# Kernel optimization log

Hardware: AMD Instinct MI355X
Metric: run time of the kernel (lower is better)

Reference implementation:

```python
import jax, jax.numpy as jnp
import numpy as np

D_MODEL = 1024
HEADS = 16
D_K = D_MODEL // HEADS
D_FF = 4 * D_MODEL
EPS = 1e-6


def setup_inputs() -> dict:
    key = jax.random.key(0)
    ks = jax.random.split(key, 8)
    B, S = 2, 2048
    x = jax.random.normal(ks[0], (B, S, D_MODEL), dtype=jnp.float32)
    mask = jnp.tril(jnp.ones((S, S), dtype=jnp.float32))  # causal mask
    sd = 1.0 / np.sqrt(D_MODEL)
    Wq = jax.random.normal(ks[1], (D_MODEL, D_MODEL), dtype=jnp.float32) * sd
    Wk = jax.random.normal(ks[2], (D_MODEL, D_MODEL), dtype=jnp.float32) * sd
    Wv = jax.random.normal(ks[3], (D_MODEL, D_MODEL), dtype=jnp.float32) * sd
    Wo = jax.random.normal(ks[4], (D_MODEL, D_MODEL), dtype=jnp.float32) * sd
    W1 = jax.random.normal(ks[5], (D_FF, D_MODEL), dtype=jnp.float32) * sd  # torch Linear weight [out,in]
    W2 = jax.random.normal(ks[6], (D_MODEL, D_FF), dtype=jnp.float32) * (1.0 / np.sqrt(D_FF))
    g1 = jnp.ones((D_MODEL,), dtype=jnp.float32)
    b1 = jnp.zeros((D_MODEL,), dtype=jnp.float32)
    g2 = jnp.ones((D_MODEL,), dtype=jnp.float32)
    b2 = jnp.zeros((D_MODEL,), dtype=jnp.float32)
    return dict(x=x, mask=mask, Wq=Wq, Wk=Wk, Wv=Wv, Wo=Wo, W1=W1, W2=W2,
                g1=g1, b1=b1, g2=g2, b2=b2)


def _layernorm(x, gamma, beta):
    mean = jnp.mean(x, axis=-1, keepdims=True)
    var = jnp.var(x, axis=-1, keepdims=True, ddof=1)  # torch.var is unbiased
    return gamma * (x - mean) / jnp.sqrt(var + EPS) + beta


def reference(x, mask, Wq, Wk, Wv, Wo, W1, W2, g1, b1, g2, b2):
    B, S, D = x.shape
    def split_heads(t):
        return t.reshape(B, S, HEADS, D_K).transpose(0, 2, 1, 3)  # [B,H,S,dk]
    q = split_heads(x @ Wq.T)
    k = split_heads(x @ Wk.T)
    v = split_heads(x @ Wv.T)
    scores = jnp.einsum('bhqd,bhkd->bhqk', q, k) / np.sqrt(D_K)
    scores = jnp.where(mask == 0, -jnp.inf, scores)
    weights = jax.nn.softmax(scores, axis=-1)
    attn = jnp.einsum('bhqk,bhkd->bhqd', weights, v)
    attn = attn.transpose(0, 2, 1, 3).reshape(B, S, D) @ Wo.T
    x = _layernorm(x + attn, g1, b1)
    ff = jax.nn.relu(x @ W1.T) @ W2.T
    return _layernorm(x + ff, g2, b2)
```

## Files before the change

### kernel.cpp

```cpp
#include <hip/hip_runtime.h>

typedef __attribute__((ext_vector_type(8))) short short8;
typedef __attribute__((ext_vector_type(4))) float f32x4;
typedef unsigned short u16;

#define DEV static __device__ __forceinline__

DEV float b2f(u16 u) { union { unsigned u; float f; } c; c.u = ((unsigned)u) << 16; return c.f; }
DEV u16 f2b(float f) {
    union { float f; unsigned u; } c; c.f = f;
    unsigned u = c.u;
    u += 0x7fffu + ((u >> 16) & 1u);
    return (u16)(u >> 16);
}

DEV float wred_sum(float v) {
    #pragma unroll
    for (int o = 32; o > 0; o >>= 1) v += __shfl_xor(v, o, 64);
    return v;
}

DEV void glds16(const u16* g, u16* l) {
    __builtin_amdgcn_global_load_lds((const __attribute__((address_space(1))) void*)g,
                                     (__attribute__((address_space(3))) void*)l, 16, 0, 0);
}

__global__ __launch_bounds__(256) void cast_all(const float* __restrict__ x,
                                                const float* __restrict__ Wq,
                                                const float* __restrict__ Wk,
                                                const float* __restrict__ Wv,
                                                const float* __restrict__ Wo,
                                                const float* __restrict__ W1,
                                                const float* __restrict__ W2,
                                                u16* __restrict__ xb,
                                                u16* __restrict__ wqkvb,
                                                u16* __restrict__ wob,
                                                u16* __restrict__ w1b,
                                                u16* __restrict__ w2b) {
    int blk = blockIdx.x;
    const float* src; u16* dst; int boff;
    if      (blk < 2048) { src = x;  dst = xb;              boff = blk; }
    else if (blk < 2560) { src = Wq; dst = wqkvb;           boff = blk - 2048; }
    else if (blk < 3072) { src = Wk; dst = wqkvb + 1048576; boff = blk - 2560; }
    else if (blk < 3584) { src = Wv; dst = wqkvb + 2097152; boff = blk - 3072; }
    else if (blk < 4096) { src = Wo; dst = wob;             boff = blk - 3584; }
    else if (blk < 6144) { src = W1; dst = w1b;             boff = blk - 4096; }
    else                 { src = W2; dst = w2b;             boff = blk - 6144; }
    int i = boff * 2048 + threadIdx.x * 8;
    float4 a = *(const float4*)(src + i);
    float4 b = *(const float4*)(src + i + 4);
    uint4 o;
    o.x = (unsigned)f2b(a.x) | ((unsigned)f2b(a.y) << 16);
    o.y = (unsigned)f2b(a.z) | ((unsigned)f2b(a.w) << 16);
    o.z = (unsigned)f2b(b.x) | ((unsigned)f2b(b.y) << 16);
    o.w = (unsigned)f2b(b.z) | ((unsigned)f2b(b.w) << 16);
    *(uint4*)(dst + i) = o;
}

template <int OUT_MODE>
__global__ __launch_bounds__(256) void gemm128(const u16* __restrict__ A,
                                               const u16* __restrict__ Bt,
                                               void* __restrict__ Cout,
                                               int M, int N, int Kd,
                                               int GMx, int GNx, int cxs) {
    __shared__ __attribute__((aligned(16))) u16 As[2][4096];
    __shared__ __attribute__((aligned(16))) u16 Bs[2][4096];

    const int tid  = threadIdx.x;
    const int wid  = tid >> 6;
    const int lane = tid & 63;
    const int quad = lane >> 4;
    const int l16  = lane & 15;
    const int wm   = wid & 1;
    const int wn   = wid >> 1;

    const int id  = blockIdx.x;
    const int xcd = id & 7;
    const int s   = id >> 3;
    const int xr  = xcd >> cxs;
    const int xc  = xcd & ((1 << cxs) - 1);
    const int nl  = s % GNx;
    const int ml  = s / GNx;
    const int m0  = (xr * GMx + ml) * 128;
    const int n0  = (xc * GNx + nl) * 128;

    const int c0 = tid, c1 = 256 + tid;
    const int mA0 = c0 >> 2, mA1 = c1 >> 2;
    const int kg0 = (c0 & 3) ^ ((mA0 ^ (mA0 >> 2)) & 3);
    const int kg1 = (c1 & 3) ^ ((mA1 ^ (mA1 >> 2)) & 3);
    const u16* ga0 = A  + (size_t)(m0 + mA0) * Kd + kg0 * 8;
    const u16* ga1 = A  + (size_t)(m0 + mA1) * Kd + kg1 * 8;
    const u16* gb0 = Bt + (size_t)(n0 + mA0) * Kd + kg0 * 8;
    const u16* gb1 = Bt + (size_t)(n0 + mA1) * Kd + kg1 * 8;

    f32x4 acc[4][4] = {};

    int mfr[4], nfr[4];
    #pragma unroll
    for (int t = 0; t < 4; ++t) {
        int m = wm * 64 + t * 16 + l16;
        mfr[t] = m * 32 + (quad ^ ((m ^ (m >> 2)) & 3)) * 8;
        int n = wn * 64 + t * 16 + l16;
        nfr[t] = n * 32 + (quad ^ ((n ^ (n >> 2)) & 3)) * 8;
    }

    #define STAGE(buf, kk)                                   \
        do {                                                 \
            glds16(ga0 + (kk), &As[buf][c0 * 8]);            \
            glds16(ga1 + (kk), &As[buf][c1 * 8]);            \
            glds16(gb0 + (kk), &Bs[buf][c0 * 8]);            \
            glds16(gb1 + (kk), &Bs[buf][c1 * 8]);            \
        } while (0)

    #define COMPUTE(buf)                                                      \
        do {                                                                  \
            short8 af[4], bf[4];                                              \
            _Pragma("unroll")                                                 \
            for (int t = 0; t < 4; ++t) af[t] = *(const short8*)&As[buf][mfr[t]]; \
            _Pragma("unroll")                                                 \
            for (int t = 0; t < 4; ++t) bf[t] = *(const short8*)&Bs[buf][nfr[t]]; \
            _Pragma("unroll")                                                 \
            for (int mt = 0; mt < 4; ++mt)                                    \
                _Pragma("unroll")                                             \
                for (int nt = 0; nt < 4; ++nt)                                \
                    acc[mt][nt] = __builtin_amdgcn_mfma_f32_16x16x32_bf16(af[mt], bf[nt], acc[mt][nt], 0, 0, 0); \
        } while (0)

    STAGE(0, 0);
    for (int k0 = 0; k0 < Kd; k0 += 64) {
        __syncthreads();
        STAGE(1, k0 + 32);
        COMPUTE(0);
        __syncthreads();
        if (k0 + 64 < Kd) STAGE(0, k0 + 64);
        COMPUTE(1);
    }
    #undef STAGE
    #undef COMPUTE

    #pragma unroll
    for (int mt = 0; mt < 4; ++mt) {
        #pragma unroll
        for (int nt = 0; nt < 4; ++nt) {
            #pragma unroll
            for (int r = 0; r < 4; ++r) {
                int row = m0 + wm * 64 + mt * 16 + quad * 4 + r;
                int col = n0 + wn * 64 + nt * 16 + l16;
                float v = acc[mt][nt][r];
                if (OUT_MODE == 1) v = fmaxf(v, 0.f);
                if (OUT_MODE == 2) {
                    ((float*)Cout)[(size_t)row * N + col] = v;
                } else {
                    ((u16*)Cout)[(size_t)row * N + col] = f2b(v);
                }
            }
        }
    }
}

#define QS 3072
__global__ __launch_bounds__(256) void attn_mfma(const u16* __restrict__ QKV,
                                                 u16* __restrict__ Om) {
    __shared__ __attribute__((aligned(16))) u16 K_sh[64][72];
    __shared__ __attribute__((aligned(16))) u16 V_sh[64][72];
    __shared__ __attribute__((aligned(16))) u16 P_sh[4][32][72];

    const int tid  = threadIdx.x;
    const int wid  = tid >> 6;
    const int lane = tid & 63;
    const int quad = lane >> 4;
    const int l16  = lane & 15;
    const int bh   = blockIdx.x & 31;
    const int b    = bh >> 4, h = bh & 15;
    const int qt   = 15 - (blockIdx.x >> 5);
    const int S = 2048, Dm = 1024;
    const int q0w = qt * 128 + wid * 32;

    const u16* Qm = QKV;
    const u16* Km = QKV + 1024;
    const u16* Vm = QKV + 2048;

    short8 bq[2][2];
    #pragma unroll
    for (int qs = 0; qs < 2; ++qs)
        #pragma unroll
        for (int dc = 0; dc < 2; ++dc)
            bq[qs][dc] = *(const short8*)(Qm + (size_t)(b * S + q0w + qs * 16 + l16) * QS
                                             + h * 64 + dc * 32 + quad * 8);

    float mS[2] = { -INFINITY, -INFINITY };
    float lS[2] = { 0.f, 0.f };
    f32x4 accO[4][2] = {};

    const int ntiles = qt * 2 + 2;
    for (int t = 0; t < ntiles; ++t) {
        const int k0 = t * 64;
        __syncthreads();
        #pragma unroll
        for (int it = 0; it < 2; ++it) {
            int key = (tid >> 3) + it * 32;
            int dcol = (tid & 7) * 8;
            *(uint4*)&K_sh[key][dcol] =
                *(const uint4*)(Km + (size_t)(b * S + k0 + key) * QS + h * 64 + dcol);
        }
        #pragma unroll
        for (int it = 0; it < 2; ++it) {
            int key = lane;
            int d0 = wid * 8 + it * 32;
            uint4 vv = *(const uint4*)(Vm + (size_t)(b * S + k0 + key) * QS + h * 64 + d0);
            const u16* ve = (const u16*)&vv;
            #pragma unroll
            for (int j = 0; j < 8; ++j) V_sh[d0 + j][key] = ve[j];
        }
        __syncthreads();

        if (k0 > q0w + 31) continue;

        f32x4 sC[4][2] = {};
        #pragma unroll
        for (int dc = 0; dc < 2; ++dc)
            #pragma unroll
            for (int st = 0; st < 4; ++st) {
                short8 ak = *(const short8*)&K_sh[st * 16 + l16][dc * 32 + quad * 8];
                #pragma unroll
                for (int qs = 0; qs < 2; ++qs)
                    sC[st][qs] = __builtin_amdgcn_mfma_f32_16x16x32_bf16(ak, bq[qs][dc], sC[st][qs], 0, 0, 0);
            }

        if (k0 + 63 > q0w) {
            #pragma unroll
            for (int st = 0; st < 4; ++st)
                #pragma unroll
                for (int qs = 0; qs < 2; ++qs)
                    #pragma unroll
                    for (int r = 0; r < 4; ++r) {
                        int key = k0 + st * 16 + quad * 4 + r;
                        int qq  = q0w + qs * 16 + l16;
                        sC[st][qs][r] = (key > qq) ? -INFINITY : sC[st][qs][r] * 0.125f;
                    }
        } else {
            #pragma unroll
            for (int st = 0; st < 4; ++st)
                #pragma unroll
                for (int qs = 0; qs < 2; ++qs)
                    #pragma unroll
                    for (int r = 0; r < 4; ++r) sC[st][qs][r] *= 0.125f;
        }

        #pragma unroll
        for (int qs = 0; qs < 2; ++qs) {
            float tmax = -INFINITY;
            #pragma unroll
            for (int st = 0; st < 4; ++st)
                #pragma unroll
                for (int r = 0; r < 4; ++r) tmax = fmaxf(tmax, sC[st][qs][r]);
            tmax = fmaxf(tmax, __shfl_xor(tmax, 16, 64));
            tmax = fmaxf(tmax, __shfl_xor(tmax, 32, 64));
            float mnew = fmaxf(mS[qs], tmax);
            float al = __expf(mS[qs] - mnew);
            mS[qs] = mnew;
            float rs = 0.f;
            #pragma unroll
            for (int st = 0; st < 4; ++st) {
                u16 pk[4];
                #pragma unroll
                for (int r = 0; r < 4; ++r) {
                    float p = __expf(sC[st][qs][r] - mnew);
                    rs += p;
                    pk[r] = f2b(p);
                }
                *(ushort4*)&P_sh[wid][qs * 16 + l16][st * 16 + quad * 4] =
                    make_ushort4(pk[0], pk[1], pk[2], pk[3]);
            }
            rs += __shfl_xor(rs, 16, 64);
            rs += __shfl_xor(rs, 32, 64);
            lS[qs] = lS[qs] * al + rs;
            #pragma unroll
            for (int dm = 0; dm < 4; ++dm)
                #pragma unroll
                for (int r = 0; r < 4; ++r) accO[dm][qs][r] *= al;
        }

        #pragma unroll
        for (int kc = 0; kc < 2; ++kc) {
            short8 bp[2];
            #pragma unroll
            for (int qs = 0; qs < 2; ++qs)
                bp[qs] = *(const short8*)&P_sh[wid][qs * 16 + l16][kc * 32 + quad * 8];
            #pragma unroll
            for (int dm = 0; dm < 4; ++dm) {
                short8 av = *(const short8*)&V_sh[dm * 16 + l16][kc * 32 + quad * 8];
                #pragma unroll
                for (int qs = 0; qs < 2; ++qs)
                    accO[dm][qs] = __builtin_amdgcn_mfma_f32_16x16x32_bf16(av, bp[qs], accO[dm][qs], 0, 0, 0);
            }
        }
    }

    __syncthreads();

    #pragma unroll
    for (int qs = 0; qs < 2; ++qs) {
        float rl = 1.f / lS[qs];
        #pragma unroll
        for (int dm = 0; dm < 4; ++dm) {
            u16 pk[4];
            #pragma unroll
            for (int r = 0; r < 4; ++r) pk[r] = f2b(accO[dm][qs][r] * rl);
            *(ushort4*)&P_sh[wid][qs * 16 + l16][dm * 16 + quad * 4] =
                make_ushort4(pk[0], pk[1], pk[2], pk[3]);
        }
    }
    __syncthreads();
    #pragma unroll
    for (int pass = 0; pass < 4; ++pass) {
        int qq = pass * 8 + (lane >> 3);
        int dd = (lane & 7) * 8;
        uint4 v = *(const uint4*)&P_sh[wid][qq][dd];
        *(uint4*)(Om + (size_t)(b * S + q0w + qq) * Dm + h * 64 + dd) = v;
    }
}

__global__ __launch_bounds__(256) void ln1_kernel(const float* __restrict__ xin,
                                                  const float* __restrict__ addf,
                                                  const float* __restrict__ g,
                                                  const float* __restrict__ bb,
                                                  float* __restrict__ x1f,
                                                  u16* __restrict__ x1b) {
    __shared__ float red[8];
    const int row = blockIdx.x, tid = threadIdx.x;
    const int wid = tid >> 6, lane = tid & 63;
    const float* xr = xin + (size_t)row * 1024;
    const float* ar = addf + (size_t)row * 1024;

    float v[4], s = 0.f, sq = 0.f;
    #pragma unroll
    for (int j = 0; j < 4; ++j) {
        int i = tid + 256 * j;
        float t = xr[i] + ar[i];
        v[j] = t; s += t; sq += t * t;
    }
    s = wred_sum(s); sq = wred_sum(sq);
    if (lane == 0) { red[wid] = s; red[4 + wid] = sq; }
    __syncthreads();
    s  = red[0] + red[1] + red[2] + red[3];
    sq = red[4] + red[5] + red[6] + red[7];

    float mean = s * (1.f / 1024.f);
    float var  = (sq - s * mean) * (1.f / 1023.f);
    float rstd = rsqrtf(var + 1e-6f);

    #pragma unroll
    for (int j = 0; j < 4; ++j) {
        int i = tid + 256 * j;
        float o = g[i] * ((v[j] - mean) * rstd) + bb[i];
        x1f[(size_t)row * 1024 + i] = o;
        x1b[(size_t)row * 1024 + i] = f2b(o);
    }
}

__global__ __launch_bounds__(256) void ln2_kernel(const float* __restrict__ x1f,
                                                  const float* __restrict__ addf,
                                                  const float* __restrict__ g,
                                                  const float* __restrict__ bb,
                                                  float* __restrict__ out) {
    __shared__ float red[8];
    const int row = blockIdx.x, tid = threadIdx.x;
    const int wid = tid >> 6, lane = tid & 63;
    const float* xr = x1f + (size_t)row * 1024;
    const float* ar = addf + (size_t)row * 1024;

    float v[4], s = 0.f, sq = 0.f;
    #pragma unroll
    for (int j = 0; j < 4; ++j) {
        int i = tid + 256 * j;
        float t = xr[i] + ar[i];
        v[j] = t; s += t; sq += t * t;
    }
    s = wred_sum(s); sq = wred_sum(sq);
    if (lane == 0) { red[wid] = s; red[4 + wid] = sq; }
    __syncthreads();
    s  = red[0] + red[1] + red[2] + red[3];
    sq = red[4] + red[5] + red[6] + red[7];

    float mean = s * (1.f / 1024.f);
    float var  = (sq - s * mean) * (1.f / 1023.f);
    float rstd = rsqrtf(var + 1e-6f);

    #pragma unroll
    for (int j = 0; j < 4; ++j) {
        int i = tid + 256 * j;
        out[(size_t)row * 1024 + i] = g[i] * ((v[j] - mean) * rstd) + bb[i];
    }
}

extern "C" void kernel_launch(void* const* d_in, const int* in_sizes, int n_in,
                              void* d_out, int out_size, void* d_ws, size_t ws_size,
                              hipStream_t stream) {
    (void)in_sizes; (void)n_in; (void)out_size; (void)ws_size;
    const float* x  = (const float*)d_in[0];
    const float* Wq = (const float*)d_in[2];
    const float* Wk = (const float*)d_in[3];
    const float* Wv = (const float*)d_in[4];
    const float* Wo = (const float*)d_in[5];
    const float* W1 = (const float*)d_in[6];
    const float* W2 = (const float*)d_in[7];
    const float* g1 = (const float*)d_in[8];
    const float* b1 = (const float*)d_in[9];
    const float* g2 = (const float*)d_in[10];
    const float* b2 = (const float*)d_in[11];
    float* out = (float*)d_out;

    char* w = (char*)d_ws;
    const size_t MB = 1024ull * 1024ull;
    u16*   xb    = (u16*)(w + 0 * MB);
    u16*   Wqkvb = (u16*)(w + 8 * MB);
    u16*   Wob   = (u16*)(w + 14 * MB);
    u16*   W1b   = (u16*)(w + 16 * MB);
    u16*   W2b   = (u16*)(w + 24 * MB);
    u16*   QKVb  = (u16*)(w + 32 * MB);
    u16*   ffb   = (u16*)(w + 32 * MB);
    u16*   attnb = (u16*)(w + 64 * MB);
    u16*   x1b   = (u16*)(w + 72 * MB);
    float* tmpf  = (float*)(w + 80 * MB);
    float* x1f   = (float*)(w + 96 * MB);

    dim3 blk(256);
    cast_all<<<8192, blk, 0, stream>>>(x, Wq, Wk, Wv, Wo, W1, W2,
                                       xb, Wqkvb, Wob, W1b, W2b);

    gemm128<0><<<768, blk, 0, stream>>>(xb, Wqkvb, QKVb, 4096, 3072, 1024, 16, 6, 2);

    attn_mfma<<<512, blk, 0, stream>>>(QKVb, attnb);

    gemm128<2><<<256, blk, 0, stream>>>(attnb, Wob, tmpf, 4096, 1024, 1024, 8, 4, 1);
    ln1_kernel<<<4096, blk, 0, stream>>>(x, tmpf, g1, b1, x1f, x1b);

    gemm128<1><<<1024, blk, 0, stream>>>(x1b, W1b, ffb, 4096, 4096, 1024, 16, 8, 2);
    gemm128<2><<<256, blk, 0, stream>>>(ffb, W2b, tmpf, 4096, 1024, 4096, 8, 4, 1);
    ln2_kernel<<<4096, blk, 0, stream>>>(x1f, tmpf, g2, b2, out);
}
```

Before: 401.1 us.

## Replace direct global-to-LDS loads with register-staged prefetch pipeline in GEMM

The GEMM main loop stops using global_load_lds direct-to-LDS copies. It now loads tiles into registers two steps ahead and writes them to LDS between compute phases. The intent is to hide global latency behind the MFMA work with deeper register prefetch. The cost is extra VGPRs (16 uint4 staging registers) and explicit LDS write instructions, which may lower occupancy or add VALU/LDS traffic.

After: 398.6 us. About the same (-0.6%).

```diff
diff --git a/kernel.cpp b/kernel.cpp
--- a/kernel.cpp
+++ b/kernel.cpp
@@ -18,11 +18,6 @@
     #pragma unroll
     for (int o = 32; o > 0; o >>= 1) v += __shfl_xor(v, o, 64);
     return v;
-}
-
-DEV void glds16(const u16* g, u16* l) {
-    __builtin_amdgcn_global_load_lds((const __attribute__((address_space(1))) void*)g,
-                                     (__attribute__((address_space(3))) void*)l, 16, 0, 0);
 }
 
 __global__ __launch_bounds__(256) void cast_all(const float* __restrict__ x,
@@ -92,6 +87,10 @@
     const u16* ga1 = A  + (size_t)(m0 + mA1) * Kd + kg1 * 8;
     const u16* gb0 = Bt + (size_t)(n0 + mA0) * Kd + kg0 * 8;
     const u16* gb1 = Bt + (size_t)(n0 + mA1) * Kd + kg1 * 8;
+    u16* const lA0 = &As[0][c0 * 8]; u16* const lA1 = &As[0][c1 * 8];
+    u16* const lB0 = &Bs[0][c0 * 8]; u16* const lB1 = &Bs[0][c1 * 8];
+    u16* const hA0 = &As[1][c0 * 8]; u16* const hA1 = &As[1][c1 * 8];
+    u16* const hB0 = &Bs[1][c0 * 8]; u16* const hB1 = &Bs[1][c1 * 8];
 
     f32x4 acc[4][4] = {};
 
@@ -103,14 +102,6 @@
         int n = wn * 64 + t * 16 + l16;
         nfr[t] = n * 32 + (quad ^ ((n ^ (n >> 2)) & 3)) * 8;
     }
-
-    #define STAGE(buf, kk)                                   \
-        do {                                                 \
-            glds16(ga0 + (kk), &As[buf][c0 * 8]);            \
-            glds16(ga1 + (kk), &As[buf][c1 * 8]);            \
-            glds16(gb0 + (kk), &Bs[buf][c0 * 8]);            \
-            glds16(gb1 + (kk), &Bs[buf][c1 * 8]);            \
-        } while (0)
 
     #define COMPUTE(buf)                                                      \
         do {                                                                  \
@@ -126,16 +117,40 @@
                     acc[mt][nt] = __builtin_amdgcn_mfma_f32_16x16x32_bf16(af[mt], bf[nt], acc[mt][nt], 0, 0, 0); \
         } while (0)
 
-    STAGE(0, 0);
-    for (int k0 = 0; k0 < Kd; k0 += 64) {
-        __syncthreads();
-        STAGE(1, k0 + 32);
+    const int NT = Kd >> 5;
+    uint4 e0, e1, e2, e3;
+    uint4 o0, o1, o2, o3;
+
+    e0 = *(const uint4*)(ga0); e1 = *(const uint4*)(ga1);
+    e2 = *(const uint4*)(gb0); e3 = *(const uint4*)(gb1);
+    *(uint4*)lA0 = e0; *(uint4*)lA1 = e1;
+    *(uint4*)lB0 = e2; *(uint4*)lB1 = e3;
+    e0 = *(const uint4*)(ga0 + 32); e1 = *(const uint4*)(ga1 + 32);
+    e2 = *(const uint4*)(gb0 + 32); e3 = *(const uint4*)(gb1 + 32);
+    __syncthreads();
+
+    for (int t = 0; t < NT; t += 2) {
+        if (t + 2 < NT) {
+            int kk = (t + 2) * 32;
+            o0 = *(const uint4*)(ga0 + kk); o1 = *(const uint4*)(ga1 + kk);
+            o2 = *(const uint4*)(gb0 + kk); o3 = *(const uint4*)(gb1 + kk);
+        }
+        *(uint4*)hA0 = e0; *(uint4*)hA1 = e1;
+        *(uint4*)hB0 = e2; *(uint4*)hB1 = e3;
         COMPUTE(0);
         __syncthreads();
-        if (k0 + 64 < Kd) STAGE(0, k0 + 64);
+        if (t + 3 < NT) {
+            int kk = (t + 3) * 32;
+            e0 = *(const uint4*)(ga0 + kk); e1 = *(const uint4*)(ga1 + kk);
+            e2 = *(const uint4*)(gb0 + kk); e3 = *(const uint4*)(gb1 + kk);
+        }
+        if (t + 2 < NT) {
+            *(uint4*)lA0 = o0; *(uint4*)lA1 = o1;
+            *(uint4*)lB0 = o2; *(uint4*)lB1 = o3;
+        }
         COMPUTE(1);
-    }
-    #undef STAGE
+        __syncthreads();
+    }
     #undef COMPUTE
 
     #pragma unroll
```
